# Kernel optimization log

Measured on AMD Instinct MI355X. Metric: run time of the kernel, lower is better.

## Reference

```python
import jax, jax.numpy as jnp
import numpy as np

D = 256
H1, H2 = 256, 128

def setup_inputs() -> dict:
    key0 = jax.random.key(0)
    ks = jax.random.split(key0, 10)
    B, Lq, Lk = 2, 512, 512
    query = jax.random.normal(ks[0], (B, Lq, D), dtype=jnp.float32)
    key_t = jax.random.normal(ks[1], (B, Lk, D), dtype=jnp.float32)
    value = jax.random.normal(ks[2], (B, Lk, D), dtype=jnp.float32)
    mask = jnp.ones((B, Lq, Lk), dtype=jnp.int32)
    s1 = 1.0 / np.sqrt(2 * D)
    W1 = jax.random.uniform(ks[3], (2 * D, H1), jnp.float32, -s1, s1)  # torch Linear(2D,H1), [in,out]
    b1 = jax.random.uniform(ks[4], (H1,), jnp.float32, -s1, s1)
    s2 = 1.0 / np.sqrt(H1)
    W2 = jax.random.uniform(ks[5], (H1, H2), jnp.float32, -s2, s2)
    b2 = jax.random.uniform(ks[6], (H2,), jnp.float32, -s2, s2)
    s3 = 1.0 / np.sqrt(H2)
    W3 = jax.random.uniform(ks[7], (H2, 1), jnp.float32, -s3, s3)
    b3 = jax.random.uniform(ks[8], (1,), jnp.float32, -s3, s3)
    return {"query": query, "key": key_t, "value": value, "mask": mask,
            "W1": W1, "b1": b1, "W2": W2, "b2": b2, "W3": W3, "b3": b3}

def reference(query, key, value, mask, W1, b1, W2, b2, W3, b3):
    # Original: cat([q_i, k_j]) @ W1 == q_i @ W1[:D] + k_j @ W1[D:]  (algebraic split,
    # identical math, avoids materializing the [B,Lq,Lk,2D] concat tensor).
    W1q, W1k = W1[:D], W1[D:]
    qp = jnp.einsum('bqd,dh->bqh', query, W1q)           # [B,Lq,H1]
    kp = jnp.einsum('bkd,dh->bkh', key, W1k)             # [B,Lk,H1]
    h1 = jax.nn.relu(qp[:, :, None, :] + kp[:, None, :, :] + b1)   # [B,Lq,Lk,H1]
    h2 = jax.nn.relu(jnp.einsum('bqkh,hj->bqkj', h1, W2) + b2)      # [B,Lq,Lk,H2]
    scores = (jnp.einsum('bqkj,jo->bqko', h2, W3) + b3)[..., 0]     # [B,Lq,Lk]
    scores = jnp.where(mask == 0, jnp.float32(-1e9), scores)
    attn = jax.nn.softmax(scores, axis=-1)               # dropout is identity in eval mode
    out = jnp.einsum('bqk,bkd->bqd', attn, value)
    return out, attn
```

## Files before the change

kernel.cpp:

```cpp
#include <hip/hip_runtime.h>

#define D_  256
#define H1_ 256
#define H2_ 128
#define B_  2
#define LQ_ 512
#define LK_ 512

typedef float  f32x4  __attribute__((ext_vector_type(4)));
typedef __bf16 bf16x8 __attribute__((ext_vector_type(8)));

__global__ __launch_bounds__(256) void prep_kernel(
    const float* __restrict__ query, const float* __restrict__ key,
    const float* __restrict__ W1, const float* __restrict__ b1,
    const float* __restrict__ W2,
    float* __restrict__ qp, float* __restrict__ kp, __bf16* __restrict__ w2f) {
  const int blk = blockIdx.x;
  const int tid = threadIdx.x;
  if (blk >= 128) {
    const int id   = (blk - 128) * 256 + tid;
    const int j    = id & 7;
    const int lane = (id >> 3) & 63;
    const int frag = id >> 9;
    const int nt = frag & 3;
    const int wn = (frag >> 2) & 1;
    const int ks = (frag >> 3) & 1;
    const int kc = frag >> 4;
    const int n = wn * 64 + nt * 16 + (lane & 15);
    const int k = kc * 64 + ks * 32 + ((lane >> 4) << 3) + j;
    w2f[id] = (__bf16)W2[k * H2_ + n];
    return;
  }
  __shared__ __align__(16) float part[16][H1_];
  const int row0 = blk * 16;
  const int sel  = row0 >> 10;
  const float* __restrict__ src = (sel ? key : query) + (row0 & 1023) * D_;
  const int hg = tid & 63;
  const int rg = (tid >> 6) & 1;
  const int kh = tid >> 7;
  const float* __restrict__ w = W1 + sel * D_ * H1_ + kh * 128 * H1_ + hg * 4;
  const float* __restrict__ x = src + rg * 8 * D_ + kh * 128;
  f32x4 acc[8];
#pragma unroll
  for (int r = 0; r < 8; ++r) acc[r] = (f32x4){0.f, 0.f, 0.f, 0.f};
  for (int dd = 0; dd < 128; dd += 4) {
    f32x4 wv[4];
#pragma unroll
    for (int i = 0; i < 4; ++i) wv[i] = *(const f32x4*)(w + (dd + i) * H1_);
#pragma unroll
    for (int r = 0; r < 8; ++r) {
      const f32x4 xv = *(const f32x4*)(x + r * D_ + dd);
#pragma unroll
      for (int i = 0; i < 4; ++i) acc[r] += xv[i] * wv[i];
    }
  }
  if (kh == 1) {
#pragma unroll
    for (int r = 0; r < 8; ++r)
      *(f32x4*)(&part[rg * 8 + r][hg * 4]) = acc[r];
  }
  __syncthreads();
  if (kh == 0) {
    float* __restrict__ dst = (sel ? kp : qp) + (row0 & 1023) * H1_;
    f32x4 bv = (f32x4){0.f, 0.f, 0.f, 0.f};
    if (!sel) bv = *(const f32x4*)(b1 + hg * 4);
#pragma unroll
    for (int r = 0; r < 8; ++r) {
      const f32x4 res = acc[r] + *(const f32x4*)(&part[rg * 8 + r][hg * 4]) + bv;
      *(f32x4*)(dst + (rg * 8 + r) * H1_ + hg * 4) = res;
    }
  }
}

__global__ __launch_bounds__(256, 2) void score_kernel(
    const float* __restrict__ qp, const float* __restrict__ kp,
    const __bf16* __restrict__ w2f,
    const float* __restrict__ b2, const float* __restrict__ W3,
    const float* __restrict__ b3, float* __restrict__ scores) {
  __shared__ __align__(16) __bf16 w2lds[H1_ * H2_];

  const int b  = blockIdx.z;
  const int q0 = blockIdx.y * 16;
  const int k0 = blockIdx.x * 16;
  const int tid  = threadIdx.x;
  const int wv   = tid >> 6;
  const int lane = tid & 63;
  const int quad = lane >> 4;
  const int l16  = lane & 15;

  {
    const f32x4* __restrict__ s4 = (const f32x4*)w2f;
    f32x4* d4 = (f32x4*)w2lds;
#pragma unroll
    for (int i = 0; i < 16; ++i)
      d4[i * 256 + tid] = s4[i * 256 + tid];
  }

  f32x4 acc[4][8];
#pragma unroll
  for (int mt = 0; mt < 4; ++mt)
#pragma unroll
    for (int nt = 0; nt < 8; ++nt)
      acc[mt][nt] = (f32x4){0.f, 0.f, 0.f, 0.f};

  const float* __restrict__ qpb = qp + (b * LQ_ + q0 + wv * 4) * H1_ + quad * 8;
  const float* __restrict__ kpb = kp + (b * LK_ + k0 + l16) * H1_ + quad * 8;

  __syncthreads();

#pragma unroll
  for (int kc = 0; kc < 4; ++kc) {
#pragma unroll
    for (int ks = 0; ks < 2; ++ks) {
      const int col = kc * 64 + ks * 32;
      const f32x4 kv0 = *(const f32x4*)(kpb + col);
      const f32x4 kv1 = *(const f32x4*)(kpb + col + 4);
      bf16x8 bfr[8];
      const __bf16* fb = w2lds + (kc * 2 + ks) * 8 * 512 + lane * 8;
#pragma unroll
      for (int nt = 0; nt < 8; ++nt)
        bfr[nt] = *(const bf16x8*)(fb + nt * 512);
#pragma unroll
      for (int mt = 0; mt < 4; ++mt) {
        const f32x4 qv0 = *(const f32x4*)(qpb + mt * H1_ + col);
        const f32x4 qv1 = *(const f32x4*)(qpb + mt * H1_ + col + 4);
        bf16x8 a;
#pragma unroll
        for (int jj = 0; jj < 4; ++jj) {
          a[jj]     = (__bf16)fmaxf(qv0[jj] + kv0[jj], 0.f);
          a[jj + 4] = (__bf16)fmaxf(qv1[jj] + kv1[jj], 0.f);
        }
#pragma unroll
        for (int nt = 0; nt < 8; ++nt)
          acc[mt][nt] = __builtin_amdgcn_mfma_f32_16x16x32_bf16(
              a, bfr[nt], acc[mt][nt], 0, 0, 0);
      }
    }
  }

  float part[4][4];
#pragma unroll
  for (int mt = 0; mt < 4; ++mt)
#pragma unroll
    for (int rg = 0; rg < 4; ++rg) part[mt][rg] = 0.f;
#pragma unroll
  for (int nt = 0; nt < 8; ++nt) {
    const int cn = (nt >> 2) * 64 + (nt & 3) * 16 + l16;
    const float b2v = b2[cn];
    const float w3v = W3[cn];
#pragma unroll
    for (int mt = 0; mt < 4; ++mt)
#pragma unroll
      for (int rg = 0; rg < 4; ++rg)
        part[mt][rg] += fmaxf(acc[mt][nt][rg] + b2v, 0.f) * w3v;
  }
#pragma unroll
  for (int off = 1; off < 16; off <<= 1)
#pragma unroll
    for (int mt = 0; mt < 4; ++mt)
#pragma unroll
      for (int rg = 0; rg < 4; ++rg)
        part[mt][rg] += __shfl_xor(part[mt][rg], off, 64);
  if (l16 == 0) {
    const float b3v = b3[0];
#pragma unroll
    for (int mt = 0; mt < 4; ++mt)
#pragma unroll
      for (int rg = 0; rg < 4; ++rg)
        scores[(b * LQ_ + q0 + wv * 4 + mt) * LK_ + k0 + quad * 4 + rg] =
            part[mt][rg] + b3v;
  }
}

__global__ __launch_bounds__(512) void smout_kernel(
    const float* __restrict__ sc, float* __restrict__ attn,
    const int* __restrict__ mask, const float* __restrict__ value,
    float* __restrict__ out) {
  const int qg = blockIdx.x, b = blockIdx.y;
  const int tid = threadIdx.x;
  __shared__ __align__(16) float a_lds[LK_][4];
  __shared__ __align__(16) f32x4 p_lds[7][4][64];
  const int row0 = b * LQ_ + qg * 4;
  const int w = tid >> 6, lane = tid & 63;
  if (w < 4) {
    const float* __restrict__ srow = sc + (row0 + w) * LK_;
    const int*  __restrict__ mrow = mask + (row0 + w) * LK_;
    float v[8];
#pragma unroll
    for (int j = 0; j < 8; ++j) {
      float s = srow[lane + j * 64];
      if (mrow[lane + j * 64] == 0) s = -1e9f;
      v[j] = s;
    }
    float m = v[0];
#pragma unroll
    for (int j = 1; j < 8; ++j) m = fmaxf(m, v[j]);
#pragma unroll
    for (int off = 32; off; off >>= 1) m = fmaxf(m, __shfl_xor(m, off, 64));
    float sum = 0.f;
#pragma unroll
    for (int j = 0; j < 8; ++j) { v[j] = __expf(v[j] - m); sum += v[j]; }
#pragma unroll
    for (int off = 32; off; off >>= 1) sum += __shfl_xor(sum, off, 64);
    const float inv = 1.f / sum;
    float* __restrict__ arow = attn + (row0 + w) * LK_;
#pragma unroll
    for (int j = 0; j < 8; ++j) {
      const float p = v[j] * inv;
      a_lds[lane + j * 64][w] = p;
      arow[lane + j * 64] = p;
    }
  }
  __syncthreads();
  const int kh2 = tid >> 6;
  const int dv  = tid & 63;
  f32x4 acc[4];
#pragma unroll
  for (int q = 0; q < 4; ++q) acc[q] = (f32x4){0.f, 0.f, 0.f, 0.f};
  const f32x4* __restrict__ vb4 = (const f32x4*)value + (b * LK_ + kh2 * 64) * 64 + dv;
#pragma unroll 4
  for (int k = 0; k < 64; ++k) {
    const f32x4 v4 = vb4[k * 64];
    const f32x4 p4 = *(const f32x4*)(&a_lds[kh2 * 64 + k][0]);
#pragma unroll
    for (int q = 0; q < 4; ++q) acc[q] += p4[q] * v4;
  }
  if (kh2 > 0) {
#pragma unroll
    for (int q = 0; q < 4; ++q) p_lds[kh2 - 1][q][dv] = acc[q];
  }
  __syncthreads();
  if (kh2 == 0) {
    f32x4* __restrict__ ob4 = (f32x4*)out + row0 * 64 + dv;
#pragma unroll
    for (int q = 0; q < 4; ++q) {
      f32x4 r = acc[q];
#pragma unroll
      for (int pp = 0; pp < 7; ++pp) r += p_lds[pp][q][dv];
      ob4[q * 64] = r;
    }
  }
}

extern "C" void kernel_launch(void* const* d_in, const int* in_sizes, int n_in,
                              void* d_out, int out_size, void* d_ws, size_t ws_size,
                              hipStream_t stream) {
  (void)in_sizes; (void)n_in; (void)out_size; (void)ws_size;
  const float* query = (const float*)d_in[0];
  const float* key   = (const float*)d_in[1];
  const float* value = (const float*)d_in[2];
  const int*   mask  = (const int*)d_in[3];
  const float* W1    = (const float*)d_in[4];
  const float* b1    = (const float*)d_in[5];
  const float* W2    = (const float*)d_in[6];
  const float* b2    = (const float*)d_in[7];
  const float* W3    = (const float*)d_in[8];
  const float* b3    = (const float*)d_in[9];

  float* out  = (float*)d_out;
  float* attn = out + B_ * LQ_ * D_;

  float*  qp  = (float*)d_ws;
  float*  kp  = qp + B_ * LQ_ * H1_;
  __bf16* w2f = (__bf16*)(kp + B_ * LK_ * H1_);
  float*  sc  = (float*)(w2f + H2_ * H1_);

  prep_kernel<<<256, 256, 0, stream>>>(query, key, W1, b1, W2, qp, kp, w2f);
  dim3 gscore(LK_ / 16, LQ_ / 16, B_);
  score_kernel<<<gscore, 256, 0, stream>>>(qp, kp, w2f, b2, W3, b3, sc);
  smout_kernel<<<dim3(128, B_), 512, 0, stream>>>(sc, attn, mask, value, out);
}
```

Measured before the change: 175.1 us.

## Amortize W2 LDS staging over four key tiles and re-split prep GEMM

Each score block now computes four consecutive 16-key tiles inside a loop, so the 64KB W2 fragment copy into LDS and the b2/W3 loads are done once per four tiles. The grid drops from 2048 to 512 blocks. The prep kernel is reorganized into 576 blocks of 512 threads: each block stages 4 input rows in LDS and each thread computes one output column, split across two K halves. This trades fewer, longer score blocks (lower parallelism per CU) for less redundant LDS fill traffic.

```diff
diff --git a/kernel.cpp b/kernel.cpp
--- a/kernel.cpp
+++ b/kernel.cpp
@@ -9,16 +9,17 @@
 
 typedef float  f32x4  __attribute__((ext_vector_type(4)));
 typedef __bf16 bf16x8 __attribute__((ext_vector_type(8)));
-
-__global__ __launch_bounds__(256) void prep_kernel(
+typedef __bf16 bf16x4 __attribute__((ext_vector_type(4)));
+
+__global__ __launch_bounds__(512) void prep_kernel(
     const float* __restrict__ query, const float* __restrict__ key,
     const float* __restrict__ W1, const float* __restrict__ b1,
     const float* __restrict__ W2,
     float* __restrict__ qp, float* __restrict__ kp, __bf16* __restrict__ w2f) {
   const int blk = blockIdx.x;
   const int tid = threadIdx.x;
-  if (blk >= 128) {
-    const int id   = (blk - 128) * 256 + tid;
+  if (blk >= 512) {
+    const int id   = (blk - 512) * 512 + tid;
     const int j    = id & 7;
     const int lane = (id >> 3) & 63;
     const int frag = id >> 9;
@@ -31,44 +32,37 @@
     w2f[id] = (__bf16)W2[k * H2_ + n];
     return;
   }
-  __shared__ __align__(16) float part[16][H1_];
-  const int row0 = blk * 16;
+  __shared__ float in_lds[4][D_];
+  __shared__ float part[4][H1_];
+  const int row0 = blk * 4;
   const int sel  = row0 >> 10;
-  const float* __restrict__ src = (sel ? key : query) + (row0 & 1023) * D_;
-  const int hg = tid & 63;
-  const int rg = (tid >> 6) & 1;
-  const int kh = tid >> 7;
-  const float* __restrict__ w = W1 + sel * D_ * H1_ + kh * 128 * H1_ + hg * 4;
-  const float* __restrict__ x = src + rg * 8 * D_ + kh * 128;
-  f32x4 acc[8];
-#pragma unroll
-  for (int r = 0; r < 8; ++r) acc[r] = (f32x4){0.f, 0.f, 0.f, 0.f};
-  for (int dd = 0; dd < 128; dd += 4) {
-    f32x4 wv[4];
-#pragma unroll
-    for (int i = 0; i < 4; ++i) wv[i] = *(const f32x4*)(w + (dd + i) * H1_);
-#pragma unroll
-    for (int r = 0; r < 8; ++r) {
-      const f32x4 xv = *(const f32x4*)(x + r * D_ + dd);
-#pragma unroll
-      for (int i = 0; i < 4; ++i) acc[r] += xv[i] * wv[i];
-    }
+  const float* __restrict__ src = sel ? key : query;
+  const int base = (row0 & 1023) * D_;
+  for (int i = tid; i < 4 * D_; i += 512)
+    in_lds[i >> 8][i & 255] = src[base + i];
+  __syncthreads();
+  const int h  = tid & 255;
+  const int kh = tid >> 8;
+  float acc[4] = {0.f, 0.f, 0.f, 0.f};
+  const float* __restrict__ w = W1 + sel * D_ * H1_ + kh * 128 * H1_ + h;
+#pragma unroll 4
+  for (int dd = 0; dd < 128; ++dd) {
+    const float wv = w[dd * H1_];
+    const int d = kh * 128 + dd;
+#pragma unroll
+    for (int r = 0; r < 4; ++r) acc[r] += in_lds[r][d] * wv;
   }
   if (kh == 1) {
 #pragma unroll
-    for (int r = 0; r < 8; ++r)
-      *(f32x4*)(&part[rg * 8 + r][hg * 4]) = acc[r];
+    for (int r = 0; r < 4; ++r) part[r][h] = acc[r];
   }
   __syncthreads();
   if (kh == 0) {
-    float* __restrict__ dst = (sel ? kp : qp) + (row0 & 1023) * H1_;
-    f32x4 bv = (f32x4){0.f, 0.f, 0.f, 0.f};
-    if (!sel) bv = *(const f32x4*)(b1 + hg * 4);
-#pragma unroll
-    for (int r = 0; r < 8; ++r) {
-      const f32x4 res = acc[r] + *(const f32x4*)(&part[rg * 8 + r][hg * 4]) + bv;
-      *(f32x4*)(dst + (rg * 8 + r) * H1_ + hg * 4) = res;
-    }
+    const float bias = sel ? 0.0f : b1[h];
+    float* __restrict__ dst = sel ? kp : qp;
+#pragma unroll
+    for (int r = 0; r < 4; ++r)
+      dst[base + r * H1_ + h] = acc[r] + part[r][h] + bias;
   }
 }
 
@@ -79,9 +73,6 @@
     const float* __restrict__ b3, float* __restrict__ scores) {
   __shared__ __align__(16) __bf16 w2lds[H1_ * H2_];
 
-  const int b  = blockIdx.z;
-  const int q0 = blockIdx.y * 16;
-  const int k0 = blockIdx.x * 16;
   const int tid  = threadIdx.x;
   const int wv   = tid >> 6;
   const int lane = tid & 63;
@@ -95,80 +86,97 @@
     for (int i = 0; i < 16; ++i)
       d4[i * 256 + tid] = s4[i * 256 + tid];
   }
-
-  f32x4 acc[4][8];
-#pragma unroll
-  for (int mt = 0; mt < 4; ++mt)
-#pragma unroll
-    for (int nt = 0; nt < 8; ++nt)
-      acc[mt][nt] = (f32x4){0.f, 0.f, 0.f, 0.f};
-
-  const float* __restrict__ qpb = qp + (b * LQ_ + q0 + wv * 4) * H1_ + quad * 8;
-  const float* __restrict__ kpb = kp + (b * LK_ + k0 + l16) * H1_ + quad * 8;
-
-  __syncthreads();
-
-#pragma unroll
-  for (int kc = 0; kc < 4; ++kc) {
-#pragma unroll
-    for (int ks = 0; ks < 2; ++ks) {
-      const int col = kc * 64 + ks * 32;
-      const f32x4 kv0 = *(const f32x4*)(kpb + col);
-      const f32x4 kv1 = *(const f32x4*)(kpb + col + 4);
-      bf16x8 bfr[8];
-      const __bf16* fb = w2lds + (kc * 2 + ks) * 8 * 512 + lane * 8;
-#pragma unroll
-      for (int nt = 0; nt < 8; ++nt)
-        bfr[nt] = *(const bf16x8*)(fb + nt * 512);
-#pragma unroll
-      for (int mt = 0; mt < 4; ++mt) {
-        const f32x4 qv0 = *(const f32x4*)(qpb + mt * H1_ + col);
-        const f32x4 qv1 = *(const f32x4*)(qpb + mt * H1_ + col + 4);
-        bf16x8 a;
-#pragma unroll
-        for (int jj = 0; jj < 4; ++jj) {
-          a[jj]     = (__bf16)fmaxf(qv0[jj] + kv0[jj], 0.f);
-          a[jj + 4] = (__bf16)fmaxf(qv1[jj] + kv1[jj], 0.f);
-        }
-#pragma unroll
-        for (int nt = 0; nt < 8; ++nt)
-          acc[mt][nt] = __builtin_amdgcn_mfma_f32_16x16x32_bf16(
-              a, bfr[nt], acc[mt][nt], 0, 0, 0);
-      }
-    }
-  }
-
-  float part[4][4];
-#pragma unroll
-  for (int mt = 0; mt < 4; ++mt)
-#pragma unroll
-    for (int rg = 0; rg < 4; ++rg) part[mt][rg] = 0.f;
+  __syncthreads();
+
+  const int bid = blockIdx.x;
+  const int b   = bid >> 8;
+  const int qt  = (bid >> 3) & 31;
+  const int ktg = bid & 7;
+  const int q0  = qt * 16;
+
+  const float* __restrict__ qpb =
+      qp + (b * LQ_ + q0 + wv * 4) * H1_ + quad * 8;
+
+  float b2c[8], w3c[8];
 #pragma unroll
   for (int nt = 0; nt < 8; ++nt) {
     const int cn = (nt >> 2) * 64 + (nt & 3) * 16 + l16;
-    const float b2v = b2[cn];
-    const float w3v = W3[cn];
+    b2c[nt] = b2[cn];
+    w3c[nt] = W3[cn];
+  }
+  const float b3v = b3[0];
+
+#pragma unroll 1
+  for (int it = 0; it < 4; ++it) {
+    const int k0 = (ktg * 4 + it) * 16;
+    const float* __restrict__ kpb =
+        kp + (b * LK_ + k0 + l16) * H1_ + quad * 8;
+
+    f32x4 acc[4][8];
 #pragma unroll
     for (int mt = 0; mt < 4; ++mt)
 #pragma unroll
-      for (int rg = 0; rg < 4; ++rg)
-        part[mt][rg] += fmaxf(acc[mt][nt][rg] + b2v, 0.f) * w3v;
-  }
-#pragma unroll
-  for (int off = 1; off < 16; off <<= 1)
+      for (int nt = 0; nt < 8; ++nt)
+        acc[mt][nt] = (f32x4){0.f, 0.f, 0.f, 0.f};
+
+#pragma unroll
+    for (int kc = 0; kc < 4; ++kc) {
+#pragma unroll
+      for (int ks = 0; ks < 2; ++ks) {
+        const int col = kc * 64 + ks * 32;
+        const f32x4 kv0 = *(const f32x4*)(kpb + col);
+        const f32x4 kv1 = *(const f32x4*)(kpb + col + 4);
+        bf16x8 bfr[8];
+        const __bf16* fb = w2lds + (kc * 2 + ks) * 8 * 512 + lane * 8;
+#pragma unroll
+        for (int nt = 0; nt < 8; ++nt)
+          bfr[nt] = *(const bf16x8*)(fb + nt * 512);
+#pragma unroll
+        for (int mt = 0; mt < 4; ++mt) {
+          const f32x4 qv0 = *(const f32x4*)(qpb + mt * H1_ + col);
+          const f32x4 qv1 = *(const f32x4*)(qpb + mt * H1_ + col + 4);
+          bf16x8 a;
+#pragma unroll
+          for (int jj = 0; jj < 4; ++jj) {
+            a[jj]     = (__bf16)fmaxf(qv0[jj] + kv0[jj], 0.f);
+            a[jj + 4] = (__bf16)fmaxf(qv1[jj] + kv1[jj], 0.f);
+          }
+#pragma unroll
+          for (int nt = 0; nt < 8; ++nt)
+            acc[mt][nt] = __builtin_amdgcn_mfma_f32_16x16x32_bf16(
+                a, bfr[nt], acc[mt][nt], 0, 0, 0);
+        }
+      }
+    }
+
+    float part[4][4];
 #pragma unroll
     for (int mt = 0; mt < 4; ++mt)
 #pragma unroll
-      for (int rg = 0; rg < 4; ++rg)
-        part[mt][rg] += __shfl_xor(part[mt][rg], off, 64);
-  if (l16 == 0) {
-    const float b3v = b3[0];
-#pragma unroll
-    for (int mt = 0; mt < 4; ++mt)
-#pragma unroll
-      for (int rg = 0; rg < 4; ++rg)
-        scores[(b * LQ_ + q0 + wv * 4 + mt) * LK_ + k0 + quad * 4 + rg] =
-            part[mt][rg] + b3v;
+      for (int rg = 0; rg < 4; ++rg) part[mt][rg] = 0.f;
+#pragma unroll
+    for (int nt = 0; nt < 8; ++nt) {
+#pragma unroll
+      for (int mt = 0; mt < 4; ++mt)
+#pragma unroll
+        for (int rg = 0; rg < 4; ++rg)
+          part[mt][rg] += fmaxf(acc[mt][nt][rg] + b2c[nt], 0.f) * w3c[nt];
+    }
+#pragma unroll
+    for (int off = 1; off < 16; off <<= 1)
+#pragma unroll
+      for (int mt = 0; mt < 4; ++mt)
+#pragma unroll
+        for (int rg = 0; rg < 4; ++rg)
+          part[mt][rg] += __shfl_xor(part[mt][rg], off, 64);
+    if (l16 == 0) {
+#pragma unroll
+      for (int mt = 0; mt < 4; ++mt)
+#pragma unroll
+        for (int rg = 0; rg < 4; ++rg)
+          scores[(b * LQ_ + q0 + wv * 4 + mt) * LK_ + k0 + quad * 4 + rg] =
+              part[mt][rg] + b3v;
+    }
   }
 }
 
@@ -265,8 +273,7 @@
   __bf16* w2f = (__bf16*)(kp + B_ * LK_ * H1_);
   float*  sc  = (float*)(w2f + H2_ * H1_);
 
-  prep_kernel<<<256, 256, 0, stream>>>(query, key, W1, b1, W2, qp, kp, w2f);
-  dim3 gscore(LK_ / 16, LQ_ / 16, B_);
-  score_kernel<<<gscore, 256, 0, stream>>>(qp, kp, w2f, b2, W3, b3, sc);
+  prep_kernel<<<576, 512, 0, stream>>>(query, key, W1, b1, W2, qp, kp, w2f);
+  score_kernel<<<512, 256, 0, stream>>>(qp, kp, w2f, b2, W3, b3, sc);
   smout_kernel<<<dim3(128, B_), 512, 0, stream>>>(sc, attn, mask, value, out);
 }
```

Measured after the change: 374.0 us. 114% more time.
